# Optimization experiments

Hardware: AMD Instinct MI355X
Metric: run time of the kernel (lower is better)

Reference implementation:

```python
import jax, jax.numpy as jnp
import numpy as np

USERS = 100001   # user_num + 1
ITEMS = 100001   # item_num + 1
N = USERS + ITEMS
E = 1_000_000    # user-item interactions (nnz = 2E after symmetrization)
D = 128
N_LAYERS = 3


def setup_inputs() -> dict:
    rng = np.random.default_rng(0)
    u = rng.integers(0, USERS, E)
    it = rng.integers(0, ITEMS, E) + USERS
    # symmetric bipartite adjacency: (user, item) and (item, user) entries
    row = np.concatenate([u, it]).astype(np.int32)
    col = np.concatenate([it, u]).astype(np.int32)
    # D^{-1/2} A D^{-1/2} normalization (deg = row sums of A, + 1e-7 as in source)
    deg = np.bincount(row, minlength=N).astype(np.float64) + 1e-7
    dinv = deg ** -0.5
    vals = (dinv[row] * dinv[col]).astype(np.float32)
    key = jax.random.key(0)
    emb = jax.random.normal(key, (N, D), dtype=jnp.float32) * 0.1
    return {
        "emb": emb,
        "edge_vals": jnp.asarray(vals),
        "edge_row": jnp.asarray(row),
        "edge_col": jnp.asarray(col),
    }


def reference(emb, edge_vals, edge_row, edge_col):
    # out[row] += val * x[col]  == torch.sparse.mm(A_norm, x)
    def spmm(x):
        msgs = x[edge_col] * edge_vals[:, None]          # [nnz, D]
        return jax.ops.segment_sum(msgs, edge_row, num_segments=N)

    acc = emb
    x = emb
    for _ in range(N_LAYERS):
        x = spmm(x)
        acc = acc + x
    mean = acc / jnp.asarray(N_LAYERS + 1, dtype=emb.dtype)  # mean over stacked layers
    return mean[:USERS], mean[USERS:]
```

## Files before the change

### kernel.cpp

```cpp
#include <hip/hip_runtime.h>
#include <hip/hip_bf16.h>

#define D 128
#define TPB 256
#define SCAN_ELEMS 2048


__device__ __forceinline__ unsigned short f2bf(float f) {
    unsigned int u = __float_as_uint(f);
    unsigned int r = ((u >> 16) & 1u) + 0x7fffu;
    return (unsigned short)((u + r) >> 16);
}

__device__ __forceinline__ float bf_lo(unsigned int u) { return __uint_as_float(u << 16); }
__device__ __forceinline__ float bf_hi(unsigned int u) { return __uint_as_float(u & 0xffff0000u); }


__global__ void k_hist(const int* __restrict__ rows, int* __restrict__ counts, int nnz) {
    int e = blockIdx.x * TPB + threadIdx.x;
    if (e < nnz) atomicAdd(&counts[rows[e]], 1);
}

__global__ void k_block_sums(const int* __restrict__ counts, int n, int* __restrict__ partials) {
    __shared__ int s[TPB];
    int base = blockIdx.x * SCAN_ELEMS;
    int sum = 0;
#pragma unroll
    for (int k = 0; k < SCAN_ELEMS / TPB; ++k) {
        int idx = base + k * TPB + threadIdx.x;
        if (idx < n) sum += counts[idx];
    }
    s[threadIdx.x] = sum;
    __syncthreads();
    for (int off = TPB / 2; off > 0; off >>= 1) {
        if (threadIdx.x < off) s[threadIdx.x] += s[threadIdx.x + off];
        __syncthreads();
    }
    if (threadIdx.x == 0) partials[blockIdx.x] = s[0];
}

__global__ void k_scan_final(const int* __restrict__ counts, const int* __restrict__ partials,
                             int nscan, int* __restrict__ row_ptr, int n) {
    __shared__ int s[TPB];
    __shared__ int sh_boff, sh_total;
    if (threadIdx.x == 0) {
        int acc = 0, mine = 0;
        for (int i = 0; i < nscan; ++i) {
            if (i == (int)blockIdx.x) mine = acc;
            acc += partials[i];
        }
        sh_boff = mine;
        sh_total = acc;
    }
    __syncthreads();
    const int PER_T = SCAN_ELEMS / TPB;
    int base = blockIdx.x * SCAN_ELEMS;
    int tbase = base + threadIdx.x * PER_T;
    int loc[PER_T];
    int tsum = 0;
#pragma unroll
    for (int k = 0; k < PER_T; ++k) {
        int idx = tbase + k;
        int v = (idx < n) ? counts[idx] : 0;
        loc[k] = tsum;
        tsum += v;
    }
    s[threadIdx.x] = tsum;
    __syncthreads();
    for (int off = 1; off < TPB; off <<= 1) {
        int v = 0;
        if (threadIdx.x >= off) v = s[threadIdx.x - off];
        __syncthreads();
        if (threadIdx.x >= off) s[threadIdx.x] += v;
        __syncthreads();
    }
    int tprefix = (threadIdx.x == 0) ? 0 : s[threadIdx.x - 1];
    int boff = sh_boff;
#pragma unroll
    for (int k = 0; k < PER_T; ++k) {
        int idx = tbase + k;
        if (idx < n) row_ptr[idx] = boff + tprefix + loc[k];
    }
    if (blockIdx.x == 0 && threadIdx.x == 0) row_ptr[n] = sh_total;
}

__global__ void k_scatter(const int* __restrict__ rows, const int* __restrict__ cols,
                          const float* __restrict__ vals, const int* __restrict__ row_ptr,
                          int* __restrict__ fill, int2* __restrict__ epack, int nnz) {
    int e = blockIdx.x * TPB + threadIdx.x;
    if (e >= nnz) return;
    int r = rows[e];
    int pos = row_ptr[r] + atomicAdd(&fill[r], 1);
    epack[pos] = make_int2(cols[e], __float_as_int(vals[e]));
}

__global__ void k_cvt(const float* __restrict__ src, unsigned int* __restrict__ dst, int n8) {
    int i = blockIdx.x * TPB + threadIdx.x;
    if (i >= n8) return;
    const float4* s4 = reinterpret_cast<const float4*>(src) + (size_t)i * 2;
    float4 a = s4[0];
    float4 b = s4[1];
    uint4 o;
    o.x = (unsigned int)f2bf(a.x) | ((unsigned int)f2bf(a.y) << 16);
    o.y = (unsigned int)f2bf(a.z) | ((unsigned int)f2bf(a.w) << 16);
    o.z = (unsigned int)f2bf(b.x) | ((unsigned int)f2bf(b.y) << 16);
    o.w = (unsigned int)f2bf(b.z) | ((unsigned int)f2bf(b.w) << 16);
    reinterpret_cast<uint4*>(dst)[i] = o;
}


__device__ __forceinline__ float2 row_gather_h(const unsigned short* __restrict__ xh,
                                               const int2* __restrict__ ep,
                                               int beg, int end, int lane) {
    float2 a0 = make_float2(0.f, 0.f), a1 = a0, a2 = a0, a3 = a0;
    int j = beg;
    for (; j + 4 <= end; j += 4) {
        int2 e0 = ep[j], e1 = ep[j + 1], e2 = ep[j + 2], e3 = ep[j + 3];
        unsigned int u0 = *(reinterpret_cast<const unsigned int*>(xh + (size_t)e0.x * D) + lane);
        unsigned int u1 = *(reinterpret_cast<const unsigned int*>(xh + (size_t)e1.x * D) + lane);
        unsigned int u2 = *(reinterpret_cast<const unsigned int*>(xh + (size_t)e2.x * D) + lane);
        unsigned int u3 = *(reinterpret_cast<const unsigned int*>(xh + (size_t)e3.x * D) + lane);
        float v0 = __int_as_float(e0.y), v1 = __int_as_float(e1.y);
        float v2 = __int_as_float(e2.y), v3 = __int_as_float(e3.y);
        a0.x += v0 * bf_lo(u0); a0.y += v0 * bf_hi(u0);
        a1.x += v1 * bf_lo(u1); a1.y += v1 * bf_hi(u1);
        a2.x += v2 * bf_lo(u2); a2.y += v2 * bf_hi(u2);
        a3.x += v3 * bf_lo(u3); a3.y += v3 * bf_hi(u3);
    }
    for (; j < end; ++j) {
        int2 e = ep[j];
        unsigned int u = *(reinterpret_cast<const unsigned int*>(xh + (size_t)e.x * D) + lane);
        float v = __int_as_float(e.y);
        a0.x += v * bf_lo(u); a0.y += v * bf_hi(u);
    }
    a0.x += a1.x + a2.x + a3.x;
    a0.y += a1.y + a2.y + a3.y;
    return a0;
}

__global__ void k_spmm_mid(const unsigned short* __restrict__ xh, const int* __restrict__ row_ptr,
                           const int2* __restrict__ epack, unsigned short* __restrict__ xnext,
                           int nrows) {
    int wave = (blockIdx.x * TPB + threadIdx.x) >> 6;
    int lane = threadIdx.x & 63;
    if (wave >= nrows) return;
    int beg = __builtin_amdgcn_readfirstlane(row_ptr[wave]);
    int end = __builtin_amdgcn_readfirstlane(row_ptr[wave + 1]);
    float2 acc = row_gather_h(xh, epack, beg, end, lane);
    unsigned int packed = (unsigned int)f2bf(acc.x) | ((unsigned int)f2bf(acc.y) << 16);
    *(reinterpret_cast<unsigned int*>(xnext + (size_t)wave * D) + lane) = packed;
}

__global__ void k_spmm_final(const unsigned short* __restrict__ x1h, const int* __restrict__ row_ptr,
                             const int2* __restrict__ epack, const float* __restrict__ emb,
                             const unsigned short* __restrict__ x0h, float* __restrict__ out,
                             int nrows) {
    int wave = (blockIdx.x * TPB + threadIdx.x) >> 6;
    int lane = threadIdx.x & 63;
    if (wave >= nrows) return;
    int beg = __builtin_amdgcn_readfirstlane(row_ptr[wave]);
    int end = __builtin_amdgcn_readfirstlane(row_ptr[wave + 1]);
    float2 acc = row_gather_h(x1h, epack, beg, end, lane);

    const size_t o = (size_t)wave * D + (size_t)lane * 2;
    float e0 = __builtin_nontemporal_load(emb + o);
    float e1 = __builtin_nontemporal_load(emb + o + 1);
    unsigned int p0 = *(reinterpret_cast<const unsigned int*>(x0h + (size_t)wave * D) + lane);
    unsigned int p1 = *(reinterpret_cast<const unsigned int*>(x1h + (size_t)wave * D) + lane);
    float r0 = (e0 + bf_lo(p0) + bf_lo(p1) + acc.x) * 0.25f;
    float r1 = (e1 + bf_hi(p0) + bf_hi(p1) + acc.y) * 0.25f;
    __builtin_nontemporal_store(r0, out + o);
    __builtin_nontemporal_store(r1, out + o + 1);
}

extern "C" void kernel_launch(void* const* d_in, const int* in_sizes, int n_in,
                              void* d_out, int out_size, void* d_ws, size_t ws_size,
                              hipStream_t stream) {
    const float* emb  = (const float*)d_in[0];
    const float* vals = (const float*)d_in[1];
    const int*   rows = (const int*)d_in[2];
    const int*   cols = (const int*)d_in[3];
    float* out = (float*)d_out;

    const int nd  = in_sizes[0];
    const int nnz = in_sizes[2];
    const int n   = nd / D;

    char* w = (char*)d_ws;
    auto alloc = [&](size_t bytes) {
        char* p = w;
        w += (bytes + 255) & ~(size_t)255;
        return p;
    };
    unsigned short* embh = (unsigned short*)alloc((size_t)nd * 2);
    unsigned short* x0h  = (unsigned short*)alloc((size_t)nd * 2);
    unsigned short* x1h  = (unsigned short*)alloc((size_t)nd * 2);
    int2*  epack   = (int2*)alloc((size_t)nnz * 8);
    int*   counts  = (int*)alloc((size_t)n * 4);
    int*   fill    = (int*)alloc((size_t)n * 4);
    int*   row_ptr = (int*)alloc((size_t)(n + 1) * 4);
    const int nscan = (n + SCAN_ELEMS - 1) / SCAN_ELEMS;
    int*   partials = (int*)alloc((size_t)nscan * 4);

    hipMemsetAsync(counts, 0, (size_t)n * 4, stream);
    hipMemsetAsync(fill,   0, (size_t)n * 4, stream);

    const int n8 = nd / 8;
    k_cvt<<<(n8 + TPB - 1) / TPB, TPB, 0, stream>>>(emb, (unsigned int*)embh, n8);

    const int gb_e = (nnz + TPB - 1) / TPB;
    k_hist<<<gb_e, TPB, 0, stream>>>(rows, counts, nnz);
    k_block_sums<<<nscan, TPB, 0, stream>>>(counts, n, partials);
    k_scan_final<<<nscan, TPB, 0, stream>>>(counts, partials, nscan, row_ptr, n);
    k_scatter<<<gb_e, TPB, 0, stream>>>(rows, cols, vals, row_ptr, fill, epack, nnz);

    const int rows_per_block = TPB / 64;
    const int gb_r = (n + rows_per_block - 1) / rows_per_block;
    k_spmm_mid<<<gb_r, TPB, 0, stream>>>(embh, row_ptr, epack, x0h, n);
    k_spmm_mid<<<gb_r, TPB, 0, stream>>>(x0h,  row_ptr, epack, x1h, n);
    k_spmm_final<<<gb_r, TPB, 0, stream>>>(x1h, row_ptr, epack, emb, x0h, out, n);
}
```

Measured before the change: 645.9 us.

## Fuse cvt with histogram, record atomic ranks, unroll gather by eight

Merges the bf16 conversion and row histogram into one launch, with the histogram saving each edge's atomic rank so scatter no longer needs a second atomic pass or a fill buffer. Edge kernels process four edges per thread with vector loads. The gather loop is unrolled to eight outstanding loads, and the final layer reads the bf16 copy of emb instead of the fp32 one. This adds a rank buffer, assumes nnz is divisible by four, and lowers precision of the emb term in the output.

```diff
diff --git a/kernel.cpp b/kernel.cpp
--- a/kernel.cpp
+++ b/kernel.cpp
@@ -11,15 +11,41 @@
     unsigned int r = ((u >> 16) & 1u) + 0x7fffu;
     return (unsigned short)((u + r) >> 16);
 }
-
 __device__ __forceinline__ float bf_lo(unsigned int u) { return __uint_as_float(u << 16); }
 __device__ __forceinline__ float bf_hi(unsigned int u) { return __uint_as_float(u & 0xffff0000u); }
 
-
-__global__ void k_hist(const int* __restrict__ rows, int* __restrict__ counts, int nnz) {
-    int e = blockIdx.x * TPB + threadIdx.x;
-    if (e < nnz) atomicAdd(&counts[rows[e]], 1);
-}
+__global__ void k_cvt_hist(const float* __restrict__ emb, uint4* __restrict__ embh4,
+                           int n8, int gc,
+                           const int* __restrict__ rows, int* __restrict__ counts,
+                           int* __restrict__ rank, int nnz4) {
+    int b = blockIdx.x;
+    if (b < gc) {
+        int i = b * TPB + threadIdx.x;
+        if (i < n8) {
+            const float4* s4 = reinterpret_cast<const float4*>(emb) + (size_t)i * 2;
+            float4 a = s4[0];
+            float4 c = s4[1];
+            uint4 o;
+            o.x = (unsigned int)f2bf(a.x) | ((unsigned int)f2bf(a.y) << 16);
+            o.y = (unsigned int)f2bf(a.z) | ((unsigned int)f2bf(a.w) << 16);
+            o.z = (unsigned int)f2bf(c.x) | ((unsigned int)f2bf(c.y) << 16);
+            o.w = (unsigned int)f2bf(c.z) | ((unsigned int)f2bf(c.w) << 16);
+            embh4[i] = o;
+        }
+    } else {
+        int i = (b - gc) * TPB + threadIdx.x;
+        if (i < nnz4) {
+            int4 r4 = reinterpret_cast<const int4*>(rows)[i];
+            int4 k;
+            k.x = atomicAdd(&counts[r4.x], 1);
+            k.y = atomicAdd(&counts[r4.y], 1);
+            k.z = atomicAdd(&counts[r4.z], 1);
+            k.w = atomicAdd(&counts[r4.w], 1);
+            reinterpret_cast<int4*>(rank)[i] = k;
+        }
+    }
+}
+
 
 __global__ void k_block_sums(const int* __restrict__ counts, int n, int* __restrict__ partials) {
     __shared__ int s[TPB];
@@ -85,27 +111,18 @@
 }
 
 __global__ void k_scatter(const int* __restrict__ rows, const int* __restrict__ cols,
-                          const float* __restrict__ vals, const int* __restrict__ row_ptr,
-                          int* __restrict__ fill, int2* __restrict__ epack, int nnz) {
-    int e = blockIdx.x * TPB + threadIdx.x;
-    if (e >= nnz) return;
-    int r = rows[e];
-    int pos = row_ptr[r] + atomicAdd(&fill[r], 1);
-    epack[pos] = make_int2(cols[e], __float_as_int(vals[e]));
-}
-
-__global__ void k_cvt(const float* __restrict__ src, unsigned int* __restrict__ dst, int n8) {
+                          const float* __restrict__ vals, const int* __restrict__ rank,
+                          const int* __restrict__ row_ptr, int2* __restrict__ epack, int nnz4) {
     int i = blockIdx.x * TPB + threadIdx.x;
-    if (i >= n8) return;
-    const float4* s4 = reinterpret_cast<const float4*>(src) + (size_t)i * 2;
-    float4 a = s4[0];
-    float4 b = s4[1];
-    uint4 o;
-    o.x = (unsigned int)f2bf(a.x) | ((unsigned int)f2bf(a.y) << 16);
-    o.y = (unsigned int)f2bf(a.z) | ((unsigned int)f2bf(a.w) << 16);
-    o.z = (unsigned int)f2bf(b.x) | ((unsigned int)f2bf(b.y) << 16);
-    o.w = (unsigned int)f2bf(b.z) | ((unsigned int)f2bf(b.w) << 16);
-    reinterpret_cast<uint4*>(dst)[i] = o;
+    if (i >= nnz4) return;
+    int4 r4 = reinterpret_cast<const int4*>(rows)[i];
+    int4 c4 = reinterpret_cast<const int4*>(cols)[i];
+    float4 v4 = reinterpret_cast<const float4*>(vals)[i];
+    int4 k4 = reinterpret_cast<const int4*>(rank)[i];
+    epack[row_ptr[r4.x] + k4.x] = make_int2(c4.x, __float_as_int(v4.x));
+    epack[row_ptr[r4.y] + k4.y] = make_int2(c4.y, __float_as_int(v4.y));
+    epack[row_ptr[r4.z] + k4.z] = make_int2(c4.z, __float_as_int(v4.z));
+    epack[row_ptr[r4.w] + k4.w] = make_int2(c4.w, __float_as_int(v4.w));
 }
 
 
@@ -113,19 +130,31 @@
                                                const int2* __restrict__ ep,
                                                int beg, int end, int lane) {
     float2 a0 = make_float2(0.f, 0.f), a1 = a0, a2 = a0, a3 = a0;
+    float2 a4 = a0, a5 = a0, a6 = a0, a7 = a0;
     int j = beg;
-    for (; j + 4 <= end; j += 4) {
-        int2 e0 = ep[j], e1 = ep[j + 1], e2 = ep[j + 2], e3 = ep[j + 3];
+    for (; j + 8 <= end; j += 8) {
+        int2 e0 = ep[j],     e1 = ep[j + 1], e2 = ep[j + 2], e3 = ep[j + 3];
+        int2 e4 = ep[j + 4], e5 = ep[j + 5], e6 = ep[j + 6], e7 = ep[j + 7];
         unsigned int u0 = *(reinterpret_cast<const unsigned int*>(xh + (size_t)e0.x * D) + lane);
         unsigned int u1 = *(reinterpret_cast<const unsigned int*>(xh + (size_t)e1.x * D) + lane);
         unsigned int u2 = *(reinterpret_cast<const unsigned int*>(xh + (size_t)e2.x * D) + lane);
         unsigned int u3 = *(reinterpret_cast<const unsigned int*>(xh + (size_t)e3.x * D) + lane);
+        unsigned int u4 = *(reinterpret_cast<const unsigned int*>(xh + (size_t)e4.x * D) + lane);
+        unsigned int u5 = *(reinterpret_cast<const unsigned int*>(xh + (size_t)e5.x * D) + lane);
+        unsigned int u6 = *(reinterpret_cast<const unsigned int*>(xh + (size_t)e6.x * D) + lane);
+        unsigned int u7 = *(reinterpret_cast<const unsigned int*>(xh + (size_t)e7.x * D) + lane);
         float v0 = __int_as_float(e0.y), v1 = __int_as_float(e1.y);
         float v2 = __int_as_float(e2.y), v3 = __int_as_float(e3.y);
+        float v4 = __int_as_float(e4.y), v5 = __int_as_float(e5.y);
+        float v6 = __int_as_float(e6.y), v7 = __int_as_float(e7.y);
         a0.x += v0 * bf_lo(u0); a0.y += v0 * bf_hi(u0);
         a1.x += v1 * bf_lo(u1); a1.y += v1 * bf_hi(u1);
         a2.x += v2 * bf_lo(u2); a2.y += v2 * bf_hi(u2);
         a3.x += v3 * bf_lo(u3); a3.y += v3 * bf_hi(u3);
+        a4.x += v4 * bf_lo(u4); a4.y += v4 * bf_hi(u4);
+        a5.x += v5 * bf_lo(u5); a5.y += v5 * bf_hi(u5);
+        a6.x += v6 * bf_lo(u6); a6.y += v6 * bf_hi(u6);
+        a7.x += v7 * bf_lo(u7); a7.y += v7 * bf_hi(u7);
     }
     for (; j < end; ++j) {
         int2 e = ep[j];
@@ -133,8 +162,13 @@
         float v = __int_as_float(e.y);
         a0.x += v * bf_lo(u); a0.y += v * bf_hi(u);
     }
-    a0.x += a1.x + a2.x + a3.x;
-    a0.y += a1.y + a2.y + a3.y;
+    a0.x += a1.x; a0.y += a1.y;
+    a2.x += a3.x; a2.y += a3.y;
+    a4.x += a5.x; a4.y += a5.y;
+    a6.x += a7.x; a6.y += a7.y;
+    a0.x += a2.x; a0.y += a2.y;
+    a4.x += a6.x; a4.y += a6.y;
+    a0.x += a4.x; a0.y += a4.y;
     return a0;
 }
 
@@ -152,7 +186,7 @@
 }
 
 __global__ void k_spmm_final(const unsigned short* __restrict__ x1h, const int* __restrict__ row_ptr,
-                             const int2* __restrict__ epack, const float* __restrict__ emb,
+                             const int2* __restrict__ epack, const unsigned short* __restrict__ embh,
                              const unsigned short* __restrict__ x0h, float* __restrict__ out,
                              int nrows) {
     int wave = (blockIdx.x * TPB + threadIdx.x) >> 6;
@@ -162,13 +196,13 @@
     int end = __builtin_amdgcn_readfirstlane(row_ptr[wave + 1]);
     float2 acc = row_gather_h(x1h, epack, beg, end, lane);
 
-    const size_t o = (size_t)wave * D + (size_t)lane * 2;
-    float e0 = __builtin_nontemporal_load(emb + o);
-    float e1 = __builtin_nontemporal_load(emb + o + 1);
-    unsigned int p0 = *(reinterpret_cast<const unsigned int*>(x0h + (size_t)wave * D) + lane);
-    unsigned int p1 = *(reinterpret_cast<const unsigned int*>(x1h + (size_t)wave * D) + lane);
-    float r0 = (e0 + bf_lo(p0) + bf_lo(p1) + acc.x) * 0.25f;
-    float r1 = (e1 + bf_hi(p0) + bf_hi(p1) + acc.y) * 0.25f;
+    const size_t row_off = (size_t)wave * D;
+    unsigned int eh = *(reinterpret_cast<const unsigned int*>(embh + row_off) + lane);
+    unsigned int p0 = *(reinterpret_cast<const unsigned int*>(x0h + row_off) + lane);
+    unsigned int p1 = *(reinterpret_cast<const unsigned int*>(x1h + row_off) + lane);
+    const size_t o = row_off + (size_t)lane * 2;
+    float r0 = (bf_lo(eh) + bf_lo(p0) + bf_lo(p1) + acc.x) * 0.25f;
+    float r1 = (bf_hi(eh) + bf_hi(p0) + bf_hi(p1) + acc.y) * 0.25f;
     __builtin_nontemporal_store(r0, out + o);
     __builtin_nontemporal_store(r1, out + o + 1);
 }
@@ -196,27 +230,27 @@
     unsigned short* x0h  = (unsigned short*)alloc((size_t)nd * 2);
     unsigned short* x1h  = (unsigned short*)alloc((size_t)nd * 2);
     int2*  epack   = (int2*)alloc((size_t)nnz * 8);
+    int*   rank    = (int*)alloc((size_t)nnz * 4);
     int*   counts  = (int*)alloc((size_t)n * 4);
-    int*   fill    = (int*)alloc((size_t)n * 4);
     int*   row_ptr = (int*)alloc((size_t)(n + 1) * 4);
     const int nscan = (n + SCAN_ELEMS - 1) / SCAN_ELEMS;
     int*   partials = (int*)alloc((size_t)nscan * 4);
 
     hipMemsetAsync(counts, 0, (size_t)n * 4, stream);
-    hipMemsetAsync(fill,   0, (size_t)n * 4, stream);
 
     const int n8 = nd / 8;
-    k_cvt<<<(n8 + TPB - 1) / TPB, TPB, 0, stream>>>(emb, (unsigned int*)embh, n8);
-
-    const int gb_e = (nnz + TPB - 1) / TPB;
-    k_hist<<<gb_e, TPB, 0, stream>>>(rows, counts, nnz);
+    const int nnz4 = nnz / 4;
+    const int gc = (n8 + TPB - 1) / TPB;
+    const int gh = (nnz4 + TPB - 1) / TPB;
+    k_cvt_hist<<<gc + gh, TPB, 0, stream>>>(emb, (uint4*)embh, n8, gc,
+                                            rows, counts, rank, nnz4);
     k_block_sums<<<nscan, TPB, 0, stream>>>(counts, n, partials);
     k_scan_final<<<nscan, TPB, 0, stream>>>(counts, partials, nscan, row_ptr, n);
-    k_scatter<<<gb_e, TPB, 0, stream>>>(rows, cols, vals, row_ptr, fill, epack, nnz);
+    k_scatter<<<gh, TPB, 0, stream>>>(rows, cols, vals, rank, row_ptr, epack, nnz4);
 
     const int rows_per_block = TPB / 64;
     const int gb_r = (n + rows_per_block - 1) / rows_per_block;
     k_spmm_mid<<<gb_r, TPB, 0, stream>>>(embh, row_ptr, epack, x0h, n);
     k_spmm_mid<<<gb_r, TPB, 0, stream>>>(x0h,  row_ptr, epack, x1h, n);
-    k_spmm_final<<<gb_r, TPB, 0, stream>>>(x1h, row_ptr, epack, emb, x0h, out, n);
-}
+    k_spmm_final<<<gb_r, TPB, 0, stream>>>(x1h, row_ptr, epack, embh, x0h, out, n);
+}
```

After: 598.8 us. -7.3%, faster.
